# Optimization experiments

Measured on AMD Instinct MI355X. Metric: run time of the kernel, lower is better.

Reference implementation:

```python
import jax, jax.numpy as jnp
import numpy as np

N = 50000      # num_nodes
R = 51         # num relations (after enrichment: inverse + self-loop)
E = 16         # emb_dim
C = 8          # num_classes
B = 40         # bases
NNZ = 1_600_000  # number of triples / nonzeros per adjacency


def setup_inputs() -> dict:
    key = jax.random.key(0)
    ks = jax.random.split(key, 7)
    # random triples (s, p, o)
    s = jax.random.randint(ks[0], (NNZ,), 0, N, dtype=jnp.int32)
    o = jax.random.randint(ks[1], (NNZ,), 0, N, dtype=jnp.int32)
    p = jax.random.randint(ks[2], (NNZ,), 0, R, dtype=jnp.int32)
    # horizontal adjacency: A_hor[s, p*N + o];  vertical: A_ver[p*N + s, o]
    hor_rows = s
    hor_cols = p * N + o
    ver_rows = p * N + s
    ver_cols = o
    # values = ones / row-sum of vertical graph (sum_sparse_rgcn normalization),
    # shared by hor and ver graphs as in the torch module
    deg = jax.ops.segment_sum(jnp.ones((NNZ,), jnp.float32), ver_rows,
                              num_segments=R * N)
    values = 1.0 / deg[ver_rows]
    # parameters (basis decomposition for both layers)
    comps1 = jax.random.normal(ks[3], (R, B), dtype=jnp.float32) * 0.05
    bases1 = jax.random.normal(ks[4], (B, N, E), dtype=jnp.float32) * 0.05
    comps2 = jax.random.normal(ks[5], (R, B), dtype=jnp.float32) * 0.05
    bases2 = jax.random.normal(ks[6], (B, E, C), dtype=jnp.float32) * 0.05
    bias1 = jnp.zeros((E,), jnp.float32)
    bias2 = jnp.zeros((C,), jnp.float32)
    return {
        'values': values, 'comps1': comps1, 'bases1': bases1,
        'comps2': comps2, 'bases2': bases2, 'bias1': bias1, 'bias2': bias2,
        'hor_rows': hor_rows, 'hor_cols': hor_cols,
        'ver_rows': ver_rows, 'ver_cols': ver_cols,
    }


def reference(values, comps1, bases1, comps2, bases2, bias1, bias2,
              hor_rows, hor_cols, ver_rows, ver_cols):
    b, n, e = bases1.shape
    r = comps1.shape[0]
    c = bases2.shape[2]
    # layer 1: basis-composed weights (r, n, e) -> flat (r*n, e)
    W1 = jnp.matmul(comps1, bases1.reshape(b, n * e)).reshape(r * n, e)
    # h = hor_graph @ W1   (sparse (n, r*n) x dense (r*n, e)) via gather+scatter
    h = jax.ops.segment_sum(values[:, None] * W1[hor_cols], hor_rows,
                            num_segments=n)          # (n, e)
    h = jax.nn.relu(h + bias1)
    # hv = ver_graph @ h   (sparse (r*n, n) x dense (n, e))
    hv = jax.ops.segment_sum(values[:, None] * h[ver_cols], ver_rows,
                             num_segments=r * n).reshape(r, n, e)
    # layer 2: basis-composed weights (r, e, c), bmm + sum over relations
    W2 = jnp.matmul(comps2, bases2.reshape(b, e * c)).reshape(r, e, c)
    out = jnp.einsum('rne,rec->nc', hv, W2) + bias2   # (n, c)
    return out
```

## Files before the change

### kernel.cpp

```cpp
#include <hip/hip_runtime.h>
#include <hip/hip_bf16.h>

constexpr int N   = 50000;
constexpr int R   = 51;
constexpr int E   = 16;
constexpr int C   = 8;
constexpr int B   = 40;
constexpr int NNZ = 1600000;

constexpr int BSH   = 6;
constexpr int BKN   = 1 << BSH;
constexpr int NB    = (N + BKN - 1) >> BSH;
constexpr int NBLK  = 784;
constexpr int CHUNK = (NNZ + NBLK - 1) / NBLK;

__global__ __launch_bounds__(256) void w1_gemm_kernel(
    const float* __restrict__ comps1, const float* __restrict__ bases1,
    float* __restrict__ W1) {
  constexpr int NC2 = N * E / 2;
  int j = blockIdx.x * blockDim.x + threadIdx.x;
  if (j >= NC2) return;
  const float2* b2 = reinterpret_cast<const float2*>(bases1);
  float2 col[B];
#pragma unroll
  for (int b = 0; b < B; ++b) col[b] = b2[b * NC2 + j];
  float2* w2p = reinterpret_cast<float2*>(W1);
#pragma unroll 1
  for (int r = 0; r < R; ++r) {
    float ax = 0.f, ay = 0.f;
#pragma unroll
    for (int b = 0; b < B; ++b) {
      float cc = comps1[r * B + b];
      ax = fmaf(cc, col[b].x, ax);
      ay = fmaf(cc, col[b].y, ay);
    }
    w2p[r * NC2 + j] = make_float2(ax, ay);
  }
}

__global__ __launch_bounds__(256) void count_kernel(
    const int* __restrict__ rows, int* __restrict__ gcount) {
  __shared__ int hist[NB];
  for (int i = threadIdx.x; i < NB; i += 256) hist[i] = 0;
  __syncthreads();
  int lo = blockIdx.x * CHUNK;
  int hi = lo + CHUNK < NNZ ? lo + CHUNK : NNZ;
  for (int i = lo + threadIdx.x; i < hi; i += 256)
    atomicAdd(&hist[rows[i] >> BSH], 1);
  __syncthreads();
  for (int i = threadIdx.x; i < NB; i += 256)
    if (hist[i]) atomicAdd(&gcount[i], hist[i]);
}

__global__ __launch_bounds__(1024) void scan_kernel(
    const int* __restrict__ gcount, int* __restrict__ gstart,
    int* __restrict__ gcursor) {
  __shared__ int buf[1024];
  int t = threadIdx.x;
  int own = (t < NB) ? gcount[t] : 0;
  buf[t] = own;
  __syncthreads();
  for (int d = 1; d < 1024; d <<= 1) {
    int v = (t >= d) ? buf[t - d] : 0;
    __syncthreads();
    buf[t] += v;
    __syncthreads();
  }
  if (t < NB) {
    int st = buf[t] - own;
    gstart[t] = st;
    gcursor[t] = st;
  }
  if (t == NB - 1) gstart[NB] = buf[t];
}

__global__ __launch_bounds__(256) void scatter_kernel(
    const int* __restrict__ rows, const int* __restrict__ cols,
    const float* __restrict__ vals, int* __restrict__ gcursor,
    int2* __restrict__ packed) {
  __shared__ int hist[NB];
  __shared__ int base[NB];
  for (int i = threadIdx.x; i < NB; i += 256) hist[i] = 0;
  __syncthreads();
  int lo = blockIdx.x * CHUNK;
  int hi = lo + CHUNK < NNZ ? lo + CHUNK : NNZ;
  for (int i = lo + threadIdx.x; i < hi; i += 256)
    atomicAdd(&hist[rows[i] >> BSH], 1);
  __syncthreads();
  for (int i = threadIdx.x; i < NB; i += 256) {
    int c = hist[i];
    base[i] = c ? atomicAdd(&gcursor[i], c) : 0;
  }
  __syncthreads();
  for (int i = threadIdx.x; i < NB; i += 256) hist[i] = 0;
  __syncthreads();
  for (int i = lo + threadIdx.x; i < hi; i += 256) {
    int s = rows[i];
    int b = s >> BSH;
    int pos = base[b] + atomicAdd(&hist[b], 1);
    packed[pos] = make_int2(((s & (BKN - 1)) << 26) | cols[i],
                            __float_as_int(vals[i]));
  }
}

__global__ void w2_gemm_kernel(const float* __restrict__ comps2,
                               const float* __restrict__ bases2,
                               float* __restrict__ W2g) {
  int i = blockIdx.x * blockDim.x + threadIdx.x;
  if (i >= R * E * C) return;
  int r = i >> 7;
  int ec = i & 127;
  float acc = 0.f;
#pragma unroll
  for (int b = 0; b < B; ++b)
    acc = fmaf(comps2[r * B + b], bases2[b * 128 + ec], acc);
  W2g[i] = acc;
}

__global__ __launch_bounds__(256) void layer1_kernel(
    const float* __restrict__ W1, const int* __restrict__ gstart,
    const int2* __restrict__ packed, const float* __restrict__ bias1,
    float* __restrict__ h) {
  __shared__ float hacc[BKN * 17];
  for (int i = threadIdx.x; i < BKN * 17; i += 256) hacc[i] = 0.f;
  __syncthreads();
  int bkt = blockIdx.x;
  int lo = gstart[bkt], hi = gstart[bkt + 1];
  const float4* W14 = reinterpret_cast<const float4*>(W1);
  for (int e = lo + threadIdx.x; e < hi; e += 256) {
    int2 pk = packed[e];
    int slo = ((unsigned)pk.x) >> 26;
    int col = pk.x & ((1 << 26) - 1);
    float v = __int_as_float(pk.y);
    float4 w0 = W14[col * 4 + 0];
    float4 w1 = W14[col * 4 + 1];
    float4 w2 = W14[col * 4 + 2];
    float4 w3 = W14[col * 4 + 3];
    float* hp = &hacc[slo * 17];
    atomicAdd(hp + 0,  v * w0.x);
    atomicAdd(hp + 1,  v * w0.y);
    atomicAdd(hp + 2,  v * w0.z);
    atomicAdd(hp + 3,  v * w0.w);
    atomicAdd(hp + 4,  v * w1.x);
    atomicAdd(hp + 5,  v * w1.y);
    atomicAdd(hp + 6,  v * w1.z);
    atomicAdd(hp + 7,  v * w1.w);
    atomicAdd(hp + 8,  v * w2.x);
    atomicAdd(hp + 9,  v * w2.y);
    atomicAdd(hp + 10, v * w2.z);
    atomicAdd(hp + 11, v * w2.w);
    atomicAdd(hp + 12, v * w3.x);
    atomicAdd(hp + 13, v * w3.y);
    atomicAdd(hp + 14, v * w3.z);
    atomicAdd(hp + 15, v * w3.w);
  }
  __syncthreads();
  for (int i = threadIdx.x; i < BKN * E; i += 256) {
    int slo = i >> 4, e = i & 15;
    int node = (bkt << BSH) + slo;
    if (node < N)
      h[node * E + e] = fmaxf(hacc[slo * 17 + e] + bias1[e], 0.f);
  }
}

__global__ __launch_bounds__(256) void layer2_kernel(
    const float* __restrict__ h, const float* __restrict__ W2g,
    const int* __restrict__ gstart, const int2* __restrict__ packed,
    const float* __restrict__ bias2, float* __restrict__ out) {
  __shared__ float w2s[R * 132];
  __shared__ float oacc[BKN * 9];
  for (int i = threadIdx.x; i < R * E * C; i += 256) {
    int p = i >> 7, ec = i & 127;
    int e = ec >> 3, c = ec & 7;
    w2s[p * 132 + c * 16 + e] = W2g[i];
  }
  for (int i = threadIdx.x; i < BKN * 9; i += 256) oacc[i] = 0.f;
  __syncthreads();
  int bkt = blockIdx.x;
  int lo = gstart[bkt], hi = gstart[bkt + 1];
  const float4* H4 = reinterpret_cast<const float4*>(h);
  for (int idx = lo + threadIdx.x; idx < hi; idx += 256) {
    int2 pk = packed[idx];
    int slo = ((unsigned)pk.x) >> 26;
    int col = pk.x & ((1 << 26) - 1);
    float v = __int_as_float(pk.y);
    int p = (int)((unsigned)col / (unsigned)N);
    int o = col - p * N;
    float4 h0 = H4[o * 4 + 0];
    float4 h1 = H4[o * 4 + 1];
    float4 h2 = H4[o * 4 + 2];
    float4 h3 = H4[o * 4 + 3];
    const float4* wp = reinterpret_cast<const float4*>(&w2s[p * 132]);
#pragma unroll
    for (int c = 0; c < 8; ++c) {
      float4 a = wp[c * 4 + 0];
      float4 bq = wp[c * 4 + 1];
      float4 cq = wp[c * 4 + 2];
      float4 dq = wp[c * 4 + 3];
      float s = h0.x * a.x + h0.y * a.y + h0.z * a.z + h0.w * a.w
              + h1.x * bq.x + h1.y * bq.y + h1.z * bq.z + h1.w * bq.w
              + h2.x * cq.x + h2.y * cq.y + h2.z * cq.z + h2.w * cq.w
              + h3.x * dq.x + h3.y * dq.y + h3.z * dq.z + h3.w * dq.w;
      atomicAdd(&oacc[slo * 9 + c], v * s);
    }
  }
  __syncthreads();
  for (int i = threadIdx.x; i < BKN * C; i += 256) {
    int slo = i >> 3, c = i & 7;
    int node = (bkt << BSH) + slo;
    if (node < N) out[node * C + c] = oacc[slo * 9 + c] + bias2[c];
  }
}

extern "C" void kernel_launch(void* const* d_in, const int* in_sizes, int n_in,
                              void* d_out, int out_size, void* d_ws, size_t ws_size,
                              hipStream_t stream) {
  const float* values  = (const float*)d_in[0];
  const float* comps1  = (const float*)d_in[1];
  const float* bases1  = (const float*)d_in[2];
  const float* comps2  = (const float*)d_in[3];
  const float* bases2  = (const float*)d_in[4];
  const float* bias1   = (const float*)d_in[5];
  const float* bias2   = (const float*)d_in[6];
  const int* hor_rows  = (const int*)d_in[7];
  const int* hor_cols  = (const int*)d_in[8];
  float* out = (float*)d_out;

  char* ws = (char*)d_ws;
  size_t off = 0;
  auto alloc = [&](size_t bytes) {
    void* p = ws + off;
    off += (bytes + 255) & ~size_t(255);
    return p;
  };
  float* W1     = (float*)alloc((size_t)R * N * E * 4);
  float* h      = (float*)alloc((size_t)N * E * 4);
  float* W2g    = (float*)alloc((size_t)R * E * C * 4);
  int*   gcount = (int*)alloc((size_t)NB * 4);
  int*   gstart = (int*)alloc((size_t)(NB + 1) * 4);
  int*   gcursor= (int*)alloc((size_t)NB * 4);
  int2*  packed = (int2*)alloc((size_t)NNZ * 8);
  (void)ws_size; (void)in_sizes; (void)n_in; (void)out_size;

  hipMemsetAsync(gcount, 0, (size_t)NB * 4, stream);

  w1_gemm_kernel<<<(N * E / 2 + 255) / 256, 256, 0, stream>>>(comps1, bases1, W1);
  count_kernel<<<NBLK, 256, 0, stream>>>(hor_rows, gcount);
  scan_kernel<<<1, 1024, 0, stream>>>(gcount, gstart, gcursor);
  scatter_kernel<<<NBLK, 256, 0, stream>>>(hor_rows, hor_cols, values, gcursor,
                                           packed);
  w2_gemm_kernel<<<(R * E * C + 255) / 256, 256, 0, stream>>>(comps2, bases2, W2g);
  layer1_kernel<<<NB, 256, 0, stream>>>(W1, gstart, packed, bias1, h);
  layer2_kernel<<<NB, 256, 0, stream>>>(h, W2g, gstart, packed, bias2, out);
}
```

Before: 622.0 us.

## Bucket edges by column, stage fp16 W1 in LDS, scatter with half2 global atomics

Edges are now sorted into buckets by column (1024 W1 rows) instead of by destination row. Each layer1 block stages its W1 slice, stored as fp16, in shared memory and scatters products to global fp16 accumulators with packed half2 atomics. Layer2 uses the same bucketing, so each block only needs one or two relations of W2, and it accumulates its output with half2 global atomics. Separate relu and bias kernels convert back to fp32. This cuts the random W1 gather traffic and halves the W1 footprint, but fp16 weights and fp16 atomic accumulation lose precision, the value's low mantissa bits are overwritten to hold row bits, and global atomic contention may rise.

Result: slower. 1.330 ms (+113.9%).

```diff
diff --git a/kernel.cpp b/kernel.cpp
--- a/kernel.cpp
+++ b/kernel.cpp
@@ -1,5 +1,6 @@
 #include <hip/hip_runtime.h>
 #include <hip/hip_bf16.h>
+#include <hip/hip_fp16.h>
 
 constexpr int N   = 50000;
 constexpr int R   = 51;
@@ -7,24 +8,27 @@
 constexpr int C   = 8;
 constexpr int B   = 40;
 constexpr int NNZ = 1600000;
-
-constexpr int BSH   = 6;
-constexpr int BKN   = 1 << BSH;
-constexpr int NB    = (N + BKN - 1) >> BSH;
-constexpr int NBLK  = 784;
-constexpr int CHUNK = (NNZ + NBLK - 1) / NBLK;
+constexpr int RN  = R * N;
+
+constexpr int CSH = 10;
+constexpr int CB  = (RN + (1 << CSH) - 1) >> CSH;
+constexpr int CMASK22 = (1 << 22) - 1;
+
+constexpr int CBLK   = 784;
+constexpr int CCHUNK = (NNZ + CBLK - 1) / CBLK;
+constexpr int SBLK   = 128;
+constexpr int SCHUNK = (NNZ + SBLK - 1) / SBLK;
 
 __global__ __launch_bounds__(256) void w1_gemm_kernel(
     const float* __restrict__ comps1, const float* __restrict__ bases1,
-    float* __restrict__ W1) {
+    unsigned* __restrict__ W1u) {
   constexpr int NC2 = N * E / 2;
-  int j = blockIdx.x * blockDim.x + threadIdx.x;
+  int j = blockIdx.x * 256 + threadIdx.x;
   if (j >= NC2) return;
   const float2* b2 = reinterpret_cast<const float2*>(bases1);
   float2 col[B];
 #pragma unroll
   for (int b = 0; b < B; ++b) col[b] = b2[b * NC2 + j];
-  float2* w2p = reinterpret_cast<float2*>(W1);
 #pragma unroll 1
   for (int r = 0; r < R; ++r) {
     float ax = 0.f, ay = 0.f;
@@ -34,21 +38,23 @@
       ax = fmaf(cc, col[b].x, ax);
       ay = fmaf(cc, col[b].y, ay);
     }
-    w2p[r * NC2 + j] = make_float2(ax, ay);
+    unsigned lo = __half_as_ushort(__float2half(ax));
+    unsigned hi = __half_as_ushort(__float2half(ay));
+    W1u[r * NC2 + j] = (hi << 16) | lo;
   }
 }
 
 __global__ __launch_bounds__(256) void count_kernel(
-    const int* __restrict__ rows, int* __restrict__ gcount) {
-  __shared__ int hist[NB];
-  for (int i = threadIdx.x; i < NB; i += 256) hist[i] = 0;
-  __syncthreads();
-  int lo = blockIdx.x * CHUNK;
-  int hi = lo + CHUNK < NNZ ? lo + CHUNK : NNZ;
+    const int* __restrict__ cols, int* __restrict__ gcount) {
+  __shared__ int hist[CB];
+  for (int i = threadIdx.x; i < CB; i += 256) hist[i] = 0;
+  __syncthreads();
+  int lo = blockIdx.x * CCHUNK;
+  int hi = lo + CCHUNK < NNZ ? lo + CCHUNK : NNZ;
   for (int i = lo + threadIdx.x; i < hi; i += 256)
-    atomicAdd(&hist[rows[i] >> BSH], 1);
-  __syncthreads();
-  for (int i = threadIdx.x; i < NB; i += 256)
+    atomicAdd(&hist[(unsigned)cols[i] >> CSH], 1);
+  __syncthreads();
+  for (int i = threadIdx.x; i < CB; i += 256)
     if (hist[i]) atomicAdd(&gcount[i], hist[i]);
 }
 
@@ -56,9 +62,13 @@
     const int* __restrict__ gcount, int* __restrict__ gstart,
     int* __restrict__ gcursor) {
   __shared__ int buf[1024];
+  constexpr int CH = (CB + 1023) / 1024;
   int t = threadIdx.x;
-  int own = (t < NB) ? gcount[t] : 0;
-  buf[t] = own;
+  int lo = t * CH;
+  int hi = lo + CH < CB ? lo + CH : CB;
+  int s = 0;
+  for (int i = lo; i < hi; ++i) s += gcount[i];
+  buf[t] = s;
   __syncthreads();
   for (int d = 1; d < 1024; d <<= 1) {
     int v = (t >= d) ? buf[t - d] : 0;
@@ -66,40 +76,43 @@
     buf[t] += v;
     __syncthreads();
   }
-  if (t < NB) {
-    int st = buf[t] - own;
-    gstart[t] = st;
-    gcursor[t] = st;
-  }
-  if (t == NB - 1) gstart[NB] = buf[t];
-}
-
-__global__ __launch_bounds__(256) void scatter_kernel(
+  int run = (t > 0) ? buf[t - 1] : 0;
+  for (int i = lo; i < hi; ++i) {
+    gstart[i] = run;
+    gcursor[i] = run;
+    run += gcount[i];
+  }
+  if (t == 1023) gstart[CB] = buf[1023];
+}
+
+__global__ __launch_bounds__(1024) void scatter_kernel(
     const int* __restrict__ rows, const int* __restrict__ cols,
     const float* __restrict__ vals, int* __restrict__ gcursor,
     int2* __restrict__ packed) {
-  __shared__ int hist[NB];
-  __shared__ int base[NB];
-  for (int i = threadIdx.x; i < NB; i += 256) hist[i] = 0;
-  __syncthreads();
-  int lo = blockIdx.x * CHUNK;
-  int hi = lo + CHUNK < NNZ ? lo + CHUNK : NNZ;
-  for (int i = lo + threadIdx.x; i < hi; i += 256)
-    atomicAdd(&hist[rows[i] >> BSH], 1);
-  __syncthreads();
-  for (int i = threadIdx.x; i < NB; i += 256) {
+  __shared__ int hist[CB];
+  __shared__ int base[CB];
+  for (int i = threadIdx.x; i < CB; i += 1024) hist[i] = 0;
+  __syncthreads();
+  int lo = blockIdx.x * SCHUNK;
+  int hi = lo + SCHUNK < NNZ ? lo + SCHUNK : NNZ;
+  for (int i = lo + threadIdx.x; i < hi; i += 1024)
+    atomicAdd(&hist[(unsigned)cols[i] >> CSH], 1);
+  __syncthreads();
+  for (int i = threadIdx.x; i < CB; i += 1024) {
     int c = hist[i];
     base[i] = c ? atomicAdd(&gcursor[i], c) : 0;
   }
   __syncthreads();
-  for (int i = threadIdx.x; i < NB; i += 256) hist[i] = 0;
-  __syncthreads();
-  for (int i = lo + threadIdx.x; i < hi; i += 256) {
-    int s = rows[i];
-    int b = s >> BSH;
+  for (int i = threadIdx.x; i < CB; i += 1024) hist[i] = 0;
+  __syncthreads();
+  for (int i = lo + threadIdx.x; i < hi; i += 1024) {
+    unsigned col = (unsigned)cols[i];
+    int b = col >> CSH;
+    unsigned s = (unsigned)rows[i];
     int pos = base[b] + atomicAdd(&hist[b], 1);
-    packed[pos] = make_int2(((s & (BKN - 1)) << 26) | cols[i],
-                            __float_as_int(vals[i]));
+    unsigned w0 = ((s & 1023u) << 22) | col;
+    unsigned w1 = (__float_as_uint(vals[i]) & ~63u) | (s >> 10);
+    packed[pos] = make_int2((int)w0, (int)w1);
   }
 }
 
@@ -118,98 +131,129 @@
 }
 
 __global__ __launch_bounds__(256) void layer1_kernel(
-    const float* __restrict__ W1, const int* __restrict__ gstart,
-    const int2* __restrict__ packed, const float* __restrict__ bias1,
+    const unsigned* __restrict__ W1u, const int* __restrict__ gstart,
+    const int2* __restrict__ packed, __half2* __restrict__ h16) {
+  __shared__ unsigned wlds[1024 * 9];
+  int bkt = blockIdx.x;
+  int rowbase = bkt << CSH;
+  int nw = (RN - rowbase) < 1024 ? (RN - rowbase) * 8 : 8192;
+  const unsigned* src = W1u + (size_t)rowbase * 8;
+  for (int i = threadIdx.x; i < nw; i += 256)
+    wlds[(i >> 3) * 9 + (i & 7)] = src[i];
+  __syncthreads();
+  int lo = gstart[bkt], hi = gstart[bkt + 1];
+  for (int e = lo + (int)threadIdx.x; e < hi; e += 256) {
+    int2 r = packed[e];
+    unsigned w0 = (unsigned)r.x, w1 = (unsigned)r.y;
+    int col = (int)(w0 & CMASK22);
+    int s = (int)((w0 >> 22) | ((w1 & 63u) << 10));
+    float v = __uint_as_float(w1 & ~63u);
+    __half2 v2 = __float2half2_rn(v);
+    int lrow = col - rowbase;
+    const unsigned* wr = &wlds[lrow * 9];
+    __half2* dst = h16 + (size_t)s * 8;
+#pragma unroll
+    for (int k = 0; k < 8; ++k) {
+      __half2 wv = *reinterpret_cast<const __half2*>(&wr[k]);
+      (void)unsafeAtomicAdd(dst + k, __hmul2(wv, v2));
+    }
+  }
+}
+
+__global__ __launch_bounds__(256) void relu_kernel(
+    const unsigned* __restrict__ h16u, const float* __restrict__ bias1,
     float* __restrict__ h) {
-  __shared__ float hacc[BKN * 17];
-  for (int i = threadIdx.x; i < BKN * 17; i += 256) hacc[i] = 0.f;
-  __syncthreads();
-  int bkt = blockIdx.x;
-  int lo = gstart[bkt], hi = gstart[bkt + 1];
-  const float4* W14 = reinterpret_cast<const float4*>(W1);
-  for (int e = lo + threadIdx.x; e < hi; e += 256) {
-    int2 pk = packed[e];
-    int slo = ((unsigned)pk.x) >> 26;
-    int col = pk.x & ((1 << 26) - 1);
-    float v = __int_as_float(pk.y);
-    float4 w0 = W14[col * 4 + 0];
-    float4 w1 = W14[col * 4 + 1];
-    float4 w2 = W14[col * 4 + 2];
-    float4 w3 = W14[col * 4 + 3];
-    float* hp = &hacc[slo * 17];
-    atomicAdd(hp + 0,  v * w0.x);
-    atomicAdd(hp + 1,  v * w0.y);
-    atomicAdd(hp + 2,  v * w0.z);
-    atomicAdd(hp + 3,  v * w0.w);
-    atomicAdd(hp + 4,  v * w1.x);
-    atomicAdd(hp + 5,  v * w1.y);
-    atomicAdd(hp + 6,  v * w1.z);
-    atomicAdd(hp + 7,  v * w1.w);
-    atomicAdd(hp + 8,  v * w2.x);
-    atomicAdd(hp + 9,  v * w2.y);
-    atomicAdd(hp + 10, v * w2.z);
-    atomicAdd(hp + 11, v * w2.w);
-    atomicAdd(hp + 12, v * w3.x);
-    atomicAdd(hp + 13, v * w3.y);
-    atomicAdd(hp + 14, v * w3.z);
-    atomicAdd(hp + 15, v * w3.w);
-  }
-  __syncthreads();
-  for (int i = threadIdx.x; i < BKN * E; i += 256) {
-    int slo = i >> 4, e = i & 15;
-    int node = (bkt << BSH) + slo;
-    if (node < N)
-      h[node * E + e] = fmaxf(hacc[slo * 17 + e] + bias1[e], 0.f);
-  }
+  int i = blockIdx.x * 256 + threadIdx.x;
+  if (i >= N * E / 8) return;
+  uint4 raw = reinterpret_cast<const uint4*>(h16u)[i];
+  int ebase = (i & 1) * 8;
+  float4 o0, o1;
+  float2 f;
+  f = __half22float2(*reinterpret_cast<__half2*>(&raw.x));
+  o0.x = fmaxf(f.x + bias1[ebase + 0], 0.f);
+  o0.y = fmaxf(f.y + bias1[ebase + 1], 0.f);
+  f = __half22float2(*reinterpret_cast<__half2*>(&raw.y));
+  o0.z = fmaxf(f.x + bias1[ebase + 2], 0.f);
+  o0.w = fmaxf(f.y + bias1[ebase + 3], 0.f);
+  f = __half22float2(*reinterpret_cast<__half2*>(&raw.z));
+  o1.x = fmaxf(f.x + bias1[ebase + 4], 0.f);
+  o1.y = fmaxf(f.y + bias1[ebase + 5], 0.f);
+  f = __half22float2(*reinterpret_cast<__half2*>(&raw.w));
+  o1.z = fmaxf(f.x + bias1[ebase + 6], 0.f);
+  o1.w = fmaxf(f.y + bias1[ebase + 7], 0.f);
+  reinterpret_cast<float4*>(h)[i * 2 + 0] = o0;
+  reinterpret_cast<float4*>(h)[i * 2 + 1] = o1;
 }
 
 __global__ __launch_bounds__(256) void layer2_kernel(
     const float* __restrict__ h, const float* __restrict__ W2g,
     const int* __restrict__ gstart, const int2* __restrict__ packed,
-    const float* __restrict__ bias2, float* __restrict__ out) {
-  __shared__ float w2s[R * 132];
-  __shared__ float oacc[BKN * 9];
-  for (int i = threadIdx.x; i < R * E * C; i += 256) {
-    int p = i >> 7, ec = i & 127;
-    int e = ec >> 3, c = ec & 7;
-    w2s[p * 132 + c * 16 + e] = W2g[i];
-  }
-  for (int i = threadIdx.x; i < BKN * 9; i += 256) oacc[i] = 0.f;
-  __syncthreads();
+    __half2* __restrict__ out16) {
+  __shared__ float w2s[2][132];
   int bkt = blockIdx.x;
+  int rowbase = bkt << CSH;
+  int p0 = rowbase / N;
+  int bound = (p0 + 1) * N;
+  {
+    int i = threadIdx.x;
+    if (i < 128) {
+      int e = i >> 3, c = i & 7;
+      w2s[0][c * 16 + e] = W2g[p0 * 128 + i];
+      if (p0 + 1 < R) w2s[1][c * 16 + e] = W2g[(p0 + 1) * 128 + i];
+      else            w2s[1][c * 16 + e] = 0.f;
+    }
+  }
+  __syncthreads();
   int lo = gstart[bkt], hi = gstart[bkt + 1];
   const float4* H4 = reinterpret_cast<const float4*>(h);
-  for (int idx = lo + threadIdx.x; idx < hi; idx += 256) {
-    int2 pk = packed[idx];
-    int slo = ((unsigned)pk.x) >> 26;
-    int col = pk.x & ((1 << 26) - 1);
-    float v = __int_as_float(pk.y);
-    int p = (int)((unsigned)col / (unsigned)N);
-    int o = col - p * N;
+  for (int e = lo + (int)threadIdx.x; e < hi; e += 256) {
+    int2 r = packed[e];
+    unsigned w0 = (unsigned)r.x, w1 = (unsigned)r.y;
+    int col = (int)(w0 & CMASK22);
+    int s = (int)((w0 >> 22) | ((w1 & 63u) << 10));
+    float v = __uint_as_float(w1 & ~63u);
+    int pi = (col >= bound) ? 1 : 0;
+    int o = col - p0 * N - pi * N;
     float4 h0 = H4[o * 4 + 0];
     float4 h1 = H4[o * 4 + 1];
     float4 h2 = H4[o * 4 + 2];
     float4 h3 = H4[o * 4 + 3];
-    const float4* wp = reinterpret_cast<const float4*>(&w2s[p * 132]);
+    const float* wp = w2s[pi];
+    float sum[8];
 #pragma unroll
     for (int c = 0; c < 8; ++c) {
-      float4 a = wp[c * 4 + 0];
-      float4 bq = wp[c * 4 + 1];
-      float4 cq = wp[c * 4 + 2];
-      float4 dq = wp[c * 4 + 3];
-      float s = h0.x * a.x + h0.y * a.y + h0.z * a.z + h0.w * a.w
-              + h1.x * bq.x + h1.y * bq.y + h1.z * bq.z + h1.w * bq.w
-              + h2.x * cq.x + h2.y * cq.y + h2.z * cq.z + h2.w * cq.w
-              + h3.x * dq.x + h3.y * dq.y + h3.z * dq.z + h3.w * dq.w;
-      atomicAdd(&oacc[slo * 9 + c], v * s);
+      const float4* wq = reinterpret_cast<const float4*>(wp + c * 16);
+      float4 a = wq[0], bq = wq[1], cq = wq[2], dq = wq[3];
+      sum[c] = v * (h0.x * a.x + h0.y * a.y + h0.z * a.z + h0.w * a.w
+                  + h1.x * bq.x + h1.y * bq.y + h1.z * bq.z + h1.w * bq.w
+                  + h2.x * cq.x + h2.y * cq.y + h2.z * cq.z + h2.w * cq.w
+                  + h3.x * dq.x + h3.y * dq.y + h3.z * dq.z + h3.w * dq.w);
     }
-  }
-  __syncthreads();
-  for (int i = threadIdx.x; i < BKN * C; i += 256) {
-    int slo = i >> 3, c = i & 7;
-    int node = (bkt << BSH) + slo;
-    if (node < N) out[node * C + c] = oacc[slo * 9 + c] + bias2[c];
-  }
+    __half2* dst = out16 + (size_t)s * 4;
+#pragma unroll
+    for (int q = 0; q < 4; ++q)
+      (void)unsafeAtomicAdd(dst + q, __floats2half2_rn(sum[2 * q], sum[2 * q + 1]));
+  }
+}
+
+__global__ __launch_bounds__(256) void out_kernel(
+    const unsigned* __restrict__ out16u, const float* __restrict__ bias2,
+    float* __restrict__ out) {
+  int i = blockIdx.x * 256 + threadIdx.x;
+  if (i >= N) return;
+  uint4 raw = reinterpret_cast<const uint4*>(out16u)[i];
+  float4 o0, o1;
+  float2 f;
+  f = __half22float2(*reinterpret_cast<__half2*>(&raw.x));
+  o0.x = f.x + bias2[0]; o0.y = f.y + bias2[1];
+  f = __half22float2(*reinterpret_cast<__half2*>(&raw.y));
+  o0.z = f.x + bias2[2]; o0.w = f.y + bias2[3];
+  f = __half22float2(*reinterpret_cast<__half2*>(&raw.z));
+  o1.x = f.x + bias2[4]; o1.y = f.y + bias2[5];
+  f = __half22float2(*reinterpret_cast<__half2*>(&raw.w));
+  o1.z = f.x + bias2[6]; o1.w = f.y + bias2[7];
+  reinterpret_cast<float4*>(out)[i * 2 + 0] = o0;
+  reinterpret_cast<float4*>(out)[i * 2 + 1] = o1;
 }
 
 extern "C" void kernel_launch(void* const* d_in, const int* in_sizes, int n_in,
@@ -233,23 +277,31 @@
     off += (bytes + 255) & ~size_t(255);
     return p;
   };
-  float* W1     = (float*)alloc((size_t)R * N * E * 4);
-  float* h      = (float*)alloc((size_t)N * E * 4);
-  float* W2g    = (float*)alloc((size_t)R * E * C * 4);
-  int*   gcount = (int*)alloc((size_t)NB * 4);
-  int*   gstart = (int*)alloc((size_t)(NB + 1) * 4);
-  int*   gcursor= (int*)alloc((size_t)NB * 4);
-  int2*  packed = (int2*)alloc((size_t)NNZ * 8);
+  unsigned* W1u    = (unsigned*)alloc((size_t)RN * 8 * 4);
+  float*    h      = (float*)alloc((size_t)N * E * 4);
+  __half2*  h16    = (__half2*)alloc((size_t)N * E * 2);
+  __half2*  out16  = (__half2*)alloc((size_t)N * C * 2);
+  float*    W2g    = (float*)alloc((size_t)R * E * C * 4);
+  int*      gcount = (int*)alloc((size_t)CB * 4);
+  int*      gstart = (int*)alloc((size_t)(CB + 1) * 4);
+  int*      gcursor= (int*)alloc((size_t)CB * 4);
+  int2*     packed = (int2*)alloc((size_t)NNZ * 8);
   (void)ws_size; (void)in_sizes; (void)n_in; (void)out_size;
 
-  hipMemsetAsync(gcount, 0, (size_t)NB * 4, stream);
-
-  w1_gemm_kernel<<<(N * E / 2 + 255) / 256, 256, 0, stream>>>(comps1, bases1, W1);
-  count_kernel<<<NBLK, 256, 0, stream>>>(hor_rows, gcount);
+  (void)hipMemsetAsync(gcount, 0, (size_t)CB * 4, stream);
+  (void)hipMemsetAsync(h16, 0, (size_t)N * E * 2, stream);
+  (void)hipMemsetAsync(out16, 0, (size_t)N * C * 2, stream);
+
+  count_kernel<<<CBLK, 256, 0, stream>>>(hor_cols, gcount);
   scan_kernel<<<1, 1024, 0, stream>>>(gcount, gstart, gcursor);
-  scatter_kernel<<<NBLK, 256, 0, stream>>>(hor_rows, hor_cols, values, gcursor,
-                                           packed);
+  scatter_kernel<<<SBLK, 1024, 0, stream>>>(hor_rows, hor_cols, values, gcursor,
+                                            packed);
   w2_gemm_kernel<<<(R * E * C + 255) / 256, 256, 0, stream>>>(comps2, bases2, W2g);
-  layer1_kernel<<<NB, 256, 0, stream>>>(W1, gstart, packed, bias1, h);
-  layer2_kernel<<<NB, 256, 0, stream>>>(h, W2g, gstart, packed, bias2, out);
-}
+  w1_gemm_kernel<<<(N * E / 2 + 255) / 256, 256, 0, stream>>>(comps1, bases1, W1u);
+  layer1_kernel<<<CB, 256, 0, stream>>>(W1u, gstart, packed, h16);
+  relu_kernel<<<(N * E / 8 + 255) / 256, 256, 0, stream>>>(
+      (const unsigned*)h16, bias1, h);
+  layer2_kernel<<<CB, 256, 0, stream>>>(h, W2g, gstart, packed, out16);
+  out_kernel<<<(N + 255) / 256, 256, 0, stream>>>(
+      (const unsigned*)out16, bias2, out);
+}
```
